# Optimization experiments

Measured on AMD Instinct MI355X. Metric: run time of the kernel, lower is better.

Reference implementation:

```python
import jax, jax.numpy as jnp
import numpy as np

EPS = 1e-5

def conv3x3(x, w, b):
    # x: [B,C,H,W], w: [O,I,3,3], padding=1 (SAME)
    y = jax.lax.conv_general_dilated(x, w, window_strides=(1, 1),
                                     padding=[(1, 1), (1, 1)],
                                     dimension_numbers=('NCHW', 'OIHW', 'NCHW'))
    return y + b[None, :, None, None]

def pool_block(x, k):
    # exact adaptive avg pool: 300 is divisible by the output size, block size k
    B, C, H, W = x.shape
    return x.reshape(B, C, H // k, k, W // k, k).mean(axis=(3, 5))

def upsample_nearest(x, k):
    # equivalent to the nested python-loop slice-assign in RIA
    return jnp.repeat(jnp.repeat(x, k, axis=2), k, axis=3)

def _conv_param(key, o, i):
    k1, k2 = jax.random.split(key)
    fan_in = i * 9
    w = jax.random.normal(k1, (o, i, 3, 3), jnp.float32) * np.sqrt(2.0 / fan_in)
    b = jax.random.normal(k2, (o,), jnp.float32) * 0.01
    return w, b

def setup_inputs() -> dict:
    key = jax.random.key(0)
    ks = jax.random.split(key, 16)
    inp = {}
    inp['im'] = jax.random.normal(ks[0], (32, 3, 300, 300), jnp.float32)
    inp['w1'], inp['b1'] = _conv_param(ks[1], 8, 3)
    inp['w2'], inp['b2'] = _conv_param(ks[2], 16, 8)
    inp['w3'], inp['b3'] = _conv_param(ks[3], 32, 16)
    inp['w4'], inp['b4'] = _conv_param(ks[4], 16, 32)
    inp['w5'], inp['b5'] = _conv_param(ks[5], 8, 16)
    inp['wc5'], inp['bc5'] = _conv_param(ks[6], 8, 16)
    inp['wc10'], inp['bc10'] = _conv_param(ks[7], 8, 16)
    inp['wc15'], inp['bc15'] = _conv_param(ks[8], 8, 16)
    inp['wg'], inp['bg'] = _conv_param(ks[9], 8, 24)
    inp['wm'], inp['bm'] = _conv_param(ks[10], 8, 24)
    inp['bn_w'] = jnp.ones((8,), jnp.float32)
    inp['bn_b'] = jnp.zeros((8,), jnp.float32)
    inp['w11'], inp['b11'] = _conv_param(ks[11], 1, 8)
    inp['gamma'] = jnp.full((1,), 0.3, jnp.float32)
    return inp

def reference(im, w1, b1, w2, b2, w3, b3, w4, b4, w5, b5,
              wc5, bc5, wc10, bc10, wc15, bc15,
              wg, bg, wm, bm, bn_w, bn_b, w11, b11, gamma):
    # attention conv chain 3->8->16->32->16->8
    x = conv3x3(im, w1, b1)
    x = conv3x3(x, w2, b2)
    x = conv3x3(x, w3, b3)
    x = conv3x3(x, w4, b4)
    x = conv3x3(x, w5, b5)  # [B,8,300,300]

    # RIA: triple-scale pooled context, nearest-upsampled and fused
    up5 = upsample_nearest(pool_block(x, 5), 5)
    up10 = upsample_nearest(pool_block(x, 10), 10)
    up15 = upsample_nearest(pool_block(x, 15), 15)
    c5 = conv3x3(jnp.concatenate([x, up5], axis=1), wc5, bc5)
    c10 = conv3x3(jnp.concatenate([x, up10], axis=1), wc10, bc10)
    c15 = conv3x3(jnp.concatenate([x, up15], axis=1), wc15, bc15)
    g_in = jnp.concatenate([c5, c10, c15], axis=1)  # [B,24,300,300]

    # gated conv (activation=None): conv(x) * sigmoid(mask_conv(x)), then BN (batch stats)
    gated = conv3x3(g_in, wg, bg) * jax.nn.sigmoid(conv3x3(g_in, wm, bm))
    mean = gated.mean(axis=(0, 2, 3), keepdims=True)
    var = gated.var(axis=(0, 2, 3), keepdims=True)
    gated = (gated - mean) * jax.lax.rsqrt(var + EPS)
    gated = gated * bn_w[None, :, None, None] + bn_b[None, :, None, None]

    # 8->1 conv, sigmoid attention map, residual gating with gamma
    att = jax.nn.sigmoid(conv3x3(gated, w11, b11))  # [B,1,300,300]
    out = gamma * (att * im) + (1.0 - gamma) * im
    return out
```

## Files before the change

### kernel.cpp

```cpp
#include <hip/hip_runtime.h>
#include <hip/hip_bf16.h>
#include <math.h>

typedef __hip_bfloat16 bf16;
typedef __attribute__((ext_vector_type(8))) __bf16 bf16x8;
typedef __attribute__((ext_vector_type(8))) unsigned short u16x8;
typedef __attribute__((ext_vector_type(4))) float f32x4;

#define H_ 300
#define W_ 300
#define HW_ 90000
#define NBATCH 32
#define NPART (NBATCH * 190)
#define NPB 95

__device__ __forceinline__ float b2f(unsigned short u) {
    return __uint_as_float((unsigned int)u << 16);
}
__device__ __forceinline__ unsigned short f2u(float v) {
    bf16 b = __float2bfloat16(v);
    return *reinterpret_cast<unsigned short*>(&b);
}
__device__ __forceinline__ float sigm(float x) { return 1.f / (1.f + __expf(-x)); }
__device__ __forceinline__ unsigned int packbf(float a, float b) {
    unsigned int r;
    asm("v_cvt_pk_bf16_f32 %0, %1, %2" : "=v"(r) : "v"(a), "v"(b));
    return r;
}
__device__ __forceinline__ void async_cp16(void* lds_base, const void* g) {
    __builtin_amdgcn_global_load_lds(
        (const __attribute__((address_space(1))) unsigned int*)g,
        (__attribute__((address_space(3))) unsigned int*)lds_base, 16, 0, 0);
}

__global__ void pack_all_k(
    const float* __restrict__ w1, const float* __restrict__ w2,
    const float* __restrict__ w3, const float* __restrict__ w4,
    const float* __restrict__ w5, const float* __restrict__ wc5,
    const float* __restrict__ wc10, const float* __restrict__ wc15,
    const float* __restrict__ wg, const float* __restrict__ wm,
    unsigned short* __restrict__ WP)
{
    const float *a = nullptr, *bsec = nullptr;
    int cs = 999, CO = 0, CI = 0, CP = 8, NS = 3, NG = 1, off = 0, special = 0;
    switch (blockIdx.x) {
        case 0: a = w2;  CO = 16; CI = 8;  CP = 8;  NS = 3; off = 0;     break;
        case 1: a = w3;  CO = 32; CI = 16; CP = 16; NS = 5; NG = 2; off = 2048;  break;
        case 2: a = w4;  CO = 16; CI = 32; CP = 32; NS = 9; off = 8192;  break;
        case 3: a = w5;  CO = 8;  CI = 16; CP = 16; NS = 5; off = 13312; break;
        case 4: special = 1; CO = 32; CI = 32; CP = 32; NS = 9; NG = 2;
                off = 16384; break;
        case 5: a = wg; bsec = wm; cs = 8; CO = 16; CI = 24; CP = 32; NS = 9;
                off = 25600; break;
        case 6: a = w1;  CO = 8;  CI = 3;  CP = 8;  NS = 3; off = 30720; break;
    }
    unsigned short* outp = WP + off;
    int TPK = 32 / CP;
    int total = NS * NG * 512;
    for (int idx = threadIdx.x; idx < total; idx += 256) {
        int j = idx & 7;
        int lane = (idx >> 3) & 63;
        int g = (idx >> 9) % NG;
        int s = idx / (512 * NG);
        int col = lane & 15, kg = lane >> 4;
        int kk = kg * 8 + j;
        int tt = kk / CP, ci = kk % CP;
        int tap = s * TPK + tt;
        float v = 0.f;
        if (special) {
            int o = ci >> 3, c8 = ci & 7;
            int convid = (g == 0) ? (col < 8 ? 0 : 1) : (col < 8 ? 2 : -1);
            if (tap < 9 && convid >= 0) {
                const float* wc = (convid == 0) ? wc5 : (convid == 1) ? wc10 : wc15;
                int colc = col & 7;
                if (o == 0) v = wc[(colc * 16 + c8) * 9 + tap];
                else if (o == convid + 1) v = wc[(colc * 16 + 8 + c8) * 9 + tap];
            }
        } else {
            int co = g * 16 + col;
            if (tap < 9 && ci < CI && co < CO)
                v = (co >= cs) ? bsec[((co - cs) * CI + ci) * 9 + tap]
                               : a[(co * CI + ci) * 9 + tap];
        }
        outp[idx] = f2u(v);
    }
}

__global__ __launch_bounds__(256) void fused12_k(
    const float* __restrict__ im, const unsigned short* __restrict__ wp1,
    const float* __restrict__ b1, const unsigned short* __restrict__ wp2,
    const float* __restrict__ b2, unsigned short* __restrict__ out)
{
    __shared__ __align__(16) unsigned short s_im[1296 * 8];
    __shared__ __align__(16) unsigned short s_x1[1156 * 8];

    int b = blockIdx.z;
    int x0 = blockIdx.x * 32, y0 = blockIdx.y * 32;
    int tid = threadIdx.x;
    int lane = tid & 63, wv = tid >> 6;
    int col = lane & 15, kg = lane >> 4;

    const float* sf = im + (size_t)b * 3 * HW_;
    bool interior = (x0 >= 2) && (x0 + 34 < W_) && (y0 >= 2) && (y0 + 34 < H_);
    if (interior) {
        const float* sf0 = sf + (size_t)(y0 - 2) * W_ + (x0 - 2);
        for (int e = tid; e < 1296; e += 256) {
            int y = e / 36;
            size_t o = (size_t)e + (size_t)y * 264;
            u16x8 v = {0, 0, 0, 0, 0, 0, 0, 0};
            v[0] = f2u(sf0[o]);
            v[1] = f2u(sf0[HW_ + o]);
            v[2] = f2u(sf0[2 * HW_ + o]);
            *(u16x8*)&s_im[e * 8] = v;
        }
    } else {
        for (int e = tid; e < 1296; e += 256) {
            int y = e / 36, x = e - y * 36;
            int gy = y0 + y - 2, gx = x0 + x - 2;
            u16x8 v = {0, 0, 0, 0, 0, 0, 0, 0};
            if (gy >= 0 && gy < H_ && gx >= 0 && gx < W_) {
                size_t o = (size_t)gy * W_ + gx;
                v[0] = f2u(sf[o]);
                v[1] = f2u(sf[HW_ + o]);
                v[2] = f2u(sf[2 * HW_ + o]);
            }
            *(u16x8*)&s_im[e * 8] = v;
        }
    }

    bf16x8 bw1[3], bw2[3];
#pragma unroll
    for (int s = 0; s < 3; ++s) {
        bw1[s] = *(const bf16x8*)&wp1[(s * 64 + lane) * 8];
        bw2[s] = *(const bf16x8*)&wp2[(s * 64 + lane) * 8];
    }

    int offs1[3], offs2[3];
#pragma unroll
    for (int s = 0; s < 3; ++s) {
        int t = s * 4 + kg;
        if (t > 8) t = 8;
        offs1[s] = ((t / 3) * 36 + (t % 3)) * 8;
        offs2[s] = ((t / 3) * 34 + (t % 3)) * 8;
    }

    float b1r[4], b2r[4];
#pragma unroll
    for (int r = 0; r < 4; ++r) {
        int co1 = kg * 4 + r;
        b1r[r] = (co1 < 8) ? b1[co1] : 0.f;
        b2r[r] = b2[kg * 4 + r];
    }

    __syncthreads();

    for (int r = wv; r < 34; r += 4) {
#pragma unroll
        for (int cg = 0; cg < 3; ++cg) {
            int base = (r * 36 + cg * 16 + col) * 8;
            f32x4 acc = {0.f, 0.f, 0.f, 0.f};
#pragma unroll
            for (int s = 0; s < 3; ++s) {
                bf16x8 a = *(const bf16x8*)&s_im[base + offs1[s]];
                acc = __builtin_amdgcn_mfma_f32_16x16x32_bf16(bw1[s], a, acc, 0, 0, 0);
            }
            int c = cg * 16 + col;
            if (kg < 2 && c < 34) {
                int gy = y0 - 1 + r, gx = x0 - 1 + c;
                bool ok = (gy >= 0) && (gy < H_) && (gx >= 0) && (gx < W_);
                float o0 = ok ? acc.x + b1r[0] : 0.f;
                float o1 = ok ? acc.y + b1r[1] : 0.f;
                float o2 = ok ? acc.z + b1r[2] : 0.f;
                float o3 = ok ? acc.w + b1r[3] : 0.f;
                uint2 st;
                st.x = packbf(o0, o1);
                st.y = packbf(o2, o3);
                *(uint2*)&s_x1[(r * 34 + c) * 8 + kg * 4] = st;
            }
        }
    }
    __syncthreads();

#pragma unroll
    for (int i = 0; i < 16; ++i) {
        int m = wv * 16 + i;
        int my = m >> 1, tx = m & 1;
        int gy = y0 + my;
        if (gy >= H_) continue;
        int base = (my * 34 + tx * 16 + col) * 8;

        f32x4 acc = {0.f, 0.f, 0.f, 0.f};
#pragma unroll
        for (int s = 0; s < 3; ++s) {
            bf16x8 a = *(const bf16x8*)&s_x1[base + offs2[s]];
            acc = __builtin_amdgcn_mfma_f32_16x16x32_bf16(bw2[s], a, acc, 0, 0, 0);
        }

        int gxx = x0 + tx * 16 + col;
        if (gxx < W_) {
            uint2 st;
            st.x = packbf(acc.x + b2r[0], acc.y + b2r[1]);
            st.y = packbf(acc.z + b2r[2], acc.w + b2r[3]);
            *(uint2*)&out[((size_t)b * HW_ + (size_t)gy * W_ + gxx) * 16 +
                          kg * 4] = st;
        }
    }
}

template <int CIN, int CINP, int COUT, int NGI, int MODE, int TH>
__global__ __launch_bounds__(256) void mfconv_k(
    const unsigned short* __restrict__ src,
    const unsigned short* __restrict__ wpack,
    const float* __restrict__ bias0, const float* __restrict__ bias1,
    unsigned short* __restrict__ out, int co_total, int co_off,
    float2* __restrict__ bnp, int img_base)
{
    constexpr int TPK = 32 / CINP;
    constexpr int NSTEP = (9 + TPK - 1) / TPK;
    constexpr int OCT = CINP / 8;
    constexpr int NPX = (TH + 2) * 34;
    constexpr int STRIDE = 256 / OCT;

    __shared__ __align__(16) unsigned short s_in[OCT * NPX * 8];

    int b = blockIdx.z;
    int x0 = blockIdx.x * 32, y0 = blockIdx.y * TH;
    int tid = threadIdx.x;
    int lane = tid & 63, wv = tid >> 6;
    bool interior = (x0 >= 1) && (x0 + 32 < W_) && (y0 >= 1) && (y0 + TH < H_);

    int oct = (OCT == 1) ? 0 : (wv % OCT);
    int phase = (OCT == 4) ? 0 : (wv / OCT);
    bool voct = (CIN == CINP) || (oct * 8 < CIN);

    {
        const unsigned short* sb = src + (size_t)b * CIN * HW_;
        if (interior) {
            if (voct) {
                const unsigned short* sb0 =
                    sb + ((size_t)(y0 - 1) * W_ + (x0 - 1)) * CIN + oct * 8;
#pragma unroll
                for (int pxb = 0; pxb < NPX; pxb += STRIDE) {
                    int base = phase * 64 + pxb;
                    if (base >= NPX) break;
                    int px = base + lane;
                    if (px < NPX) {
                        int y = px / 34;
                        async_cp16(&s_in[(oct * NPX + base) * 8],
                                   &sb0[(size_t)(px + y * 266) * CIN]);
                    }
                }
            } else {
                u16x8 z8 = {0, 0, 0, 0, 0, 0, 0, 0};
                for (int px = lane + phase * 64; px < NPX; px += STRIDE)
                    *(u16x8*)&s_in[(oct * NPX + px) * 8] = z8;
            }
        } else {
            for (int px = lane + phase * 64; px < NPX; px += STRIDE) {
                int y = px / 34, x = px - y * 34;
                int gy = y0 + y - 1, gx = x0 + x - 1;
                u16x8 v = {0, 0, 0, 0, 0, 0, 0, 0};
                if (gy >= 0 && gy < H_ && gx >= 0 && gx < W_ && voct)
                    v = *(const u16x8*)&sb[((size_t)gy * W_ + gx) * CIN + oct * 8];
                *(u16x8*)&s_in[(oct * NPX + px) * 8] = v;
            }
        }
    }

    bf16x8 bw[NGI][NSTEP];
#pragma unroll
    for (int gi = 0; gi < NGI; ++gi)
#pragma unroll
        for (int s = 0; s < NSTEP; ++s)
            bw[gi][s] = *(const bf16x8*)&wpack[((s * NGI + gi) * 64 + lane) * 8];

    int col = lane & 15, kg = lane >> 4;

    float bias_r[NGI][4];
#pragma unroll
    for (int gi = 0; gi < NGI; ++gi)
#pragma unroll
        for (int r = 0; r < 4; ++r) {
            if (MODE == 2)
                bias_r[0][r] = (kg < 2) ? bias0[kg * 4 + r] : bias1[(kg - 2) * 4 + r];
            else {
                int co_l = gi * 16 + kg * 4 + r;
                bias_r[gi][r] = (co_l < COUT) ? bias0[co_l] : 0.f;
            }
        }

    float bs[4] = {0.f, 0.f, 0.f, 0.f}, bs2[4] = {0.f, 0.f, 0.f, 0.f};

    __syncthreads();

    if constexpr (OCT == 4) {
        int myb = wv * (TH / 4);
#pragma unroll
        for (int tx = 0; tx < 2; ++tx) {
            int pbase = kg * NPX + tx * 16 + col;
            bf16x8 fr[3][3];
#pragma unroll
            for (int r = 0; r < 2; ++r)
#pragma unroll
                for (int dx = 0; dx < 3; ++dx)
                    fr[r][dx] =
                        *(const bf16x8*)&s_in[(pbase + (myb + r) * 34 + dx) * 8];
#pragma unroll
            for (int ii = 0; ii < TH / 4; ++ii) {
#pragma unroll
                for (int dx = 0; dx < 3; ++dx)
                    fr[(ii + 2) % 3][dx] =
                        *(const bf16x8*)&s_in[(pbase + (myb + ii + 2) * 34 + dx) * 8];

                f32x4 acc[NGI];
#pragma unroll
                for (int gi = 0; gi < NGI; ++gi) acc[gi] = {0.f, 0.f, 0.f, 0.f};
#pragma unroll
                for (int dy = 0; dy < 3; ++dy)
#pragma unroll
                    for (int dx = 0; dx < 3; ++dx) {
                        bf16x8 a = fr[(ii + dy) % 3][dx];
#pragma unroll
                        for (int gi = 0; gi < NGI; ++gi)
                            acc[gi] = __builtin_amdgcn_mfma_f32_16x16x32_bf16(
                                bw[gi][dy * 3 + dx], a, acc[gi], 0, 0, 0);
                    }

                int gy = y0 + myb + ii;
                int gxx = x0 + tx * 16 + col;
                if (gy < H_) {
                    if (MODE == 2) {
                        float v0 = acc[0].x + bias_r[0][0];
                        float v1 = acc[0].y + bias_r[0][1];
                        float v2 = acc[0].z + bias_r[0][2];
                        float v3 = acc[0].w + bias_r[0][3];
                        float m0 = __shfl_xor(v0, 32), m1 = __shfl_xor(v1, 32);
                        float m2 = __shfl_xor(v2, 32), m3 = __shfl_xor(v3, 32);
                        if (kg < 2 && gxx < W_) {
                            float o0 = v0 * sigm(m0), o1 = v1 * sigm(m1);
                            float o2 = v2 * sigm(m2), o3 = v3 * sigm(m3);
                            uint2 st;
                            st.x = packbf(o0, o1);
                            st.y = packbf(o2, o3);
                            *(uint2*)&out[(((size_t)b * HW_ + (size_t)gy * W_ +
                                            gxx) * 8) + kg * 4] = st;
                            bs[0] += o0; bs2[0] += o0 * o0;
                            bs[1] += o1; bs2[1] += o1 * o1;
                            bs[2] += o2; bs2[2] += o2 * o2;
                            bs[3] += o3; bs2[3] += o3 * o3;
                        }
                    } else {
#pragma unroll
                        for (int gi = 0; gi < NGI; ++gi) {
                            int co_g = gi * 16 + kg * 4;
                            if (co_g < COUT && gxx < W_) {
                                uint2 st;
                                st.x = packbf(acc[gi].x + bias_r[gi][0],
                                              acc[gi].y + bias_r[gi][1]);
                                st.y = packbf(acc[gi].z + bias_r[gi][2],
                                              acc[gi].w + bias_r[gi][3]);
                                *(uint2*)&out[((size_t)b * HW_ +
                                               (size_t)gy * W_ + gxx) *
                                                  co_total + co_off + co_g] = st;
                            }
                        }
                    }
                }
            }
        }
    } else {
        int offs[NSTEP];
#pragma unroll
        for (int s = 0; s < NSTEP; ++s) {
            int t = s * TPK + kg / OCT;
            if (t > 8) t = 8;
            offs[s] = ((t / 3) * 34 + (t % 3)) * 8 + (kg % OCT) * (NPX * 8);
        }

#pragma unroll
        for (int i = 0; i < TH / 2; ++i) {
            int m = wv * (TH / 2) + i;
            int my = m >> 1, tx = m & 1;
            int gy = y0 + my;
            if (gy >= H_) continue;
            int base = (my * 34 + tx * 16 + col) * 8;

            f32x4 acc[NGI];
#pragma unroll
            for (int gi = 0; gi < NGI; ++gi) acc[gi] = {0.f, 0.f, 0.f, 0.f};
#pragma unroll
            for (int s = 0; s < NSTEP; ++s) {
                bf16x8 a = *(const bf16x8*)&s_in[base + offs[s]];
#pragma unroll
                for (int gi = 0; gi < NGI; ++gi)
                    acc[gi] = __builtin_amdgcn_mfma_f32_16x16x32_bf16(
                        bw[gi][s], a, acc[gi], 0, 0, 0);
            }

            int gxx = x0 + tx * 16 + col;
#pragma unroll
            for (int gi = 0; gi < NGI; ++gi) {
                int co_g = gi * 16 + kg * 4;
                if (co_g < COUT && gxx < W_) {
                    uint2 st;
                    st.x = packbf(acc[gi].x + bias_r[gi][0],
                                  acc[gi].y + bias_r[gi][1]);
                    st.y = packbf(acc[gi].z + bias_r[gi][2],
                                  acc[gi].w + bias_r[gi][3]);
                    *(uint2*)&out[((size_t)b * HW_ + (size_t)gy * W_ + gxx) *
                                      co_total + co_off + co_g] = st;
                }
            }
        }
    }

    if constexpr (MODE == 2) {
#pragma unroll
        for (int off = 1; off < 16; off <<= 1) {
#pragma unroll
            for (int r = 0; r < 4; ++r) {
                bs[r] += __shfl_xor(bs[r], off);
                bs2[r] += __shfl_xor(bs2[r], off);
            }
        }
        __shared__ float bsum[4][8], bsq[4][8];
        if (lane == 0) {
#pragma unroll
            for (int r = 0; r < 4; ++r) { bsum[wv][r] = bs[r]; bsq[wv][r] = bs2[r]; }
        }
        if (lane == 16) {
#pragma unroll
            for (int r = 0; r < 4; ++r) {
                bsum[wv][4 + r] = bs[r];
                bsq[wv][4 + r] = bs2[r];
            }
        }
        __syncthreads();
        if (tid < 8) {
            float s = 0.f, s2 = 0.f;
#pragma unroll
            for (int w = 0; w < 4; ++w) { s += bsum[w][tid]; s2 += bsq[w][tid]; }
            int bIdx = (img_base + b) * 190 + blockIdx.y * 10 + blockIdx.x;
            bnp[(size_t)bIdx * 8 + tid] = make_float2(s, s2);
        }
    }
}

__global__ __launch_bounds__(256) void convc3_k(
    const unsigned short* __restrict__ src,
    const unsigned short* __restrict__ p5, const unsigned short* __restrict__ p10,
    const unsigned short* __restrict__ p15,
    const unsigned short* __restrict__ wpack,
    const float* __restrict__ bc5, const float* __restrict__ bc10,
    const float* __restrict__ bc15, unsigned short* __restrict__ out)
{
    constexpr int TH = 16;
    constexpr int NPX = (TH + 2) * 34;
    __shared__ __align__(16) unsigned short s_in[4 * NPX * 8];

    int b = blockIdx.z;
    int x0 = blockIdx.x * 32, y0 = blockIdx.y * TH;
    int tid = threadIdx.x;
    int lane = tid & 63, wv = tid >> 6;
    bool interior = (x0 >= 1) && (x0 + 32 < W_) && (y0 >= 1) && (y0 + TH < H_);

    const unsigned short* sb = src + (size_t)b * 8 * HW_;
    const unsigned short* pb5 = p5 + (size_t)b * 8 * 3600;
    const unsigned short* pb10 = p10 + (size_t)b * 8 * 900;
    const unsigned short* pb15 = p15 + (size_t)b * 8 * 400;

    int oct = wv;
    if (interior) {
        if (oct == 0) {
            const unsigned short* sb0 =
                sb + ((size_t)(y0 - 1) * W_ + (x0 - 1)) * 8;
#pragma unroll
            for (int base = 0; base < NPX; base += 64) {
                int px = base + lane;
                if (px < NPX) {
                    int y = px / 34;
                    async_cp16(&s_in[(size_t)base * 8],
                               &sb0[(size_t)(px + y * 266) * 8]);
                }
            }
        } else {
            for (int px = lane; px < NPX; px += 64) {
                int y = px / 34, x = px - y * 34;
                int gy = y0 - 1 + y, gx = x0 - 1 + x;
                const unsigned short* pp =
                    (oct == 1) ? &pb5[((size_t)(gy / 5) * 60 + gx / 5) * 8]
                    : (oct == 2) ? &pb10[((size_t)(gy / 10) * 30 + gx / 10) * 8]
                                 : &pb15[((size_t)(gy / 15) * 20 + gx / 15) * 8];
                *(u16x8*)&s_in[(oct * NPX + px) * 8] = *(const u16x8*)pp;
            }
        }
    } else {
        for (int px = lane; px < NPX; px += 64) {
            int y = px / 34, x = px - y * 34;
            int gy = y0 + y - 1, gx = x0 + x - 1;
            u16x8 v = {0, 0, 0, 0, 0, 0, 0, 0};
            if (gy >= 0 && gy < H_ && gx >= 0 && gx < W_) {
                if (oct == 0)
                    v = *(const u16x8*)&sb[((size_t)gy * W_ + gx) * 8];
                else if (oct == 1)
                    v = *(const u16x8*)&pb5[((size_t)(gy / 5) * 60 + gx / 5) * 8];
                else if (oct == 2)
                    v = *(const u16x8*)&pb10[((size_t)(gy / 10) * 30 + gx / 10) * 8];
                else
                    v = *(const u16x8*)&pb15[((size_t)(gy / 15) * 20 + gx / 15) * 8];
            }
            *(u16x8*)&s_in[(oct * NPX + px) * 8] = v;
        }
    }

    bf16x8 bw[2][9];
#pragma unroll
    for (int g = 0; g < 2; ++g)
#pragma unroll
        for (int s = 0; s < 9; ++s)
            bw[g][s] = *(const bf16x8*)&wpack[((s * 2 + g) * 64 + lane) * 8];

    int col = lane & 15, kg = lane >> 4;
    float bias_r[2][4];
#pragma unroll
    for (int r = 0; r < 4; ++r) {
        bias_r[0][r] = (kg < 2) ? bc5[kg * 4 + r] : bc10[(kg - 2) * 4 + r];
        bias_r[1][r] = (kg < 2) ? bc15[kg * 4 + r] : 0.f;
    }

    __syncthreads();

    int myb = wv * (TH / 4);
#pragma unroll
    for (int tx = 0; tx < 2; ++tx) {
        int pbase = kg * NPX + tx * 16 + col;
        bf16x8 fr[3][3];
#pragma unroll
        for (int r = 0; r < 2; ++r)
#pragma unroll
            for (int dx = 0; dx < 3; ++dx)
                fr[r][dx] = *(const bf16x8*)&s_in[(pbase + (myb + r) * 34 + dx) * 8];
#pragma unroll
        for (int ii = 0; ii < TH / 4; ++ii) {
#pragma unroll
            for (int dx = 0; dx < 3; ++dx)
                fr[(ii + 2) % 3][dx] =
                    *(const bf16x8*)&s_in[(pbase + (myb + ii + 2) * 34 + dx) * 8];

            f32x4 acc[2];
            acc[0] = {0.f, 0.f, 0.f, 0.f};
            acc[1] = {0.f, 0.f, 0.f, 0.f};
#pragma unroll
            for (int dy = 0; dy < 3; ++dy)
#pragma unroll
                for (int dx = 0; dx < 3; ++dx) {
                    bf16x8 a = fr[(ii + dy) % 3][dx];
                    acc[0] = __builtin_amdgcn_mfma_f32_16x16x32_bf16(
                        bw[0][dy * 3 + dx], a, acc[0], 0, 0, 0);
                    acc[1] = __builtin_amdgcn_mfma_f32_16x16x32_bf16(
                        bw[1][dy * 3 + dx], a, acc[1], 0, 0, 0);
                }

            int gy = y0 + myb + ii;
            int gxx = x0 + tx * 16 + col;
            if (gy < H_ && gxx < W_) {
                size_t pxo = ((size_t)b * HW_ + (size_t)gy * W_ + gxx) * 24;
                uint2 st0;
                st0.x = packbf(acc[0].x + bias_r[0][0], acc[0].y + bias_r[0][1]);
                st0.y = packbf(acc[0].z + bias_r[0][2], acc[0].w + bias_r[0][3]);
                *(uint2*)&out[pxo + kg * 4] = st0;
                if (kg < 2) {
                    uint2 st1;
                    st1.x = packbf(acc[1].x + bias_r[1][0], acc[1].y + bias_r[1][1]);
                    st1.y = packbf(acc[1].z + bias_r[1][2], acc[1].w + bias_r[1][3]);
                    *(uint2*)&out[pxo + 16 + kg * 4] = st1;
                }
            }
        }
    }
}

__global__ __launch_bounds__(256) void pool5_k(const unsigned short* __restrict__ x,
                                               unsigned short* __restrict__ p5,
                                               int n)
{
    int idx = blockIdx.x * 256 + threadIdx.x;
    if (idx >= n) return;
    int b = idx / 3600;
    int rem = idx - b * 3600;
    int i = rem / 60, j = rem - i * 60;
    const unsigned short* src =
        x + ((size_t)b * HW_ + (size_t)(i * 5) * W_ + j * 5) * 8;
    float ss[8] = {0, 0, 0, 0, 0, 0, 0, 0};
#pragma unroll
    for (int r = 0; r < 5; ++r)
#pragma unroll
        for (int c = 0; c < 5; ++c) {
            u16x8 v = *(const u16x8*)&src[((size_t)r * W_ + c) * 8];
#pragma unroll
            for (int k = 0; k < 8; ++k) ss[k] += b2f(v[k]);
        }
    uint4 st;
    st.x = packbf(ss[0] * 0.04f, ss[1] * 0.04f);
    st.y = packbf(ss[2] * 0.04f, ss[3] * 0.04f);
    st.z = packbf(ss[4] * 0.04f, ss[5] * 0.04f);
    st.w = packbf(ss[6] * 0.04f, ss[7] * 0.04f);
    *(uint4*)&p5[(size_t)idx * 8] = st;
}

template <int R, int OD>
__device__ __forceinline__ void poolr_body(const unsigned short* __restrict__ p5,
                                           unsigned short* __restrict__ po, int idx)
{
    int b = idx / (OD * OD);
    int rem = idx - b * OD * OD;
    int i = rem / OD, j = rem - i * OD;
    const unsigned short* src =
        p5 + ((size_t)b * 3600 + (size_t)(i * R) * 60 + j * R) * 8;
    float ss[8] = {0, 0, 0, 0, 0, 0, 0, 0};
    const float inv = 1.f / (R * R);
#pragma unroll
    for (int r = 0; r < R; ++r)
#pragma unroll
        for (int c = 0; c < R; ++c) {
            u16x8 v = *(const u16x8*)&src[((size_t)r * 60 + c) * 8];
#pragma unroll
            for (int k = 0; k < 8; ++k) ss[k] += b2f(v[k]);
        }
    uint4 st;
    st.x = packbf(ss[0] * inv, ss[1] * inv);
    st.y = packbf(ss[2] * inv, ss[3] * inv);
    st.z = packbf(ss[4] * inv, ss[5] * inv);
    st.w = packbf(ss[6] * inv, ss[7] * inv);
    *(uint4*)&po[(size_t)idx * 8] = st;
}

__global__ __launch_bounds__(256) void poolrs_k(const unsigned short* __restrict__ p5,
                                                unsigned short* __restrict__ p10,
                                                unsigned short* __restrict__ p15,
                                                int n10, int n15)
{
    int idx = blockIdx.x * 256 + threadIdx.x;
    if (idx < n10) {
        poolr_body<2, 30>(p5, p10, idx);
    } else {
        idx -= n10;
        if (idx < n15) poolr_body<3, 20>(p5, p15, idx);
    }
}

__global__ __launch_bounds__(256) void reduce_parts_k(
    const float2* __restrict__ parts, float2* __restrict__ parts2)
{
    int k = blockIdx.x;
    int tid = threadIdx.x;
    int c = tid & 7, j = tid >> 3;
    float s = 0.f, s2 = 0.f;
    for (int r = j; r < NPB; r += 32) {
        float2 p = parts[((size_t)k * NPB + r) * 8 + c];
        s += p.x;
        s2 += p.y;
    }
    __shared__ float2 red[256];
    red[tid] = make_float2(s, s2);
    __syncthreads();
    if (tid < 8) {
        float a = 0.f, b = 0.f;
        for (int q = 0; q < 32; ++q) {
            float2 p = red[q * 8 + tid];
            a += p.x;
            b += p.y;
        }
        parts2[(size_t)k * 8 + tid] = make_float2(a, b);
    }
}

__global__ __launch_bounds__(256) void stats_fold_k(
    const float2* __restrict__ parts2, const float* __restrict__ bn_w,
    const float* __restrict__ bn_b, const float* __restrict__ w11,
    const float* __restrict__ b11, float* __restrict__ wfold)
{
    __shared__ float sc[8], tc[8];
    __shared__ float2 acc8[8];
    int tid = threadIdx.x;
    int c = tid >> 5, sl = tid & 31;
    float s = 0.f, s2 = 0.f;
    for (int i = sl; i < 64; i += 32) {
        float2 p = parts2[(size_t)i * 8 + c];
        s += p.x;
        s2 += p.y;
    }
#pragma unroll
    for (int off = 16; off > 0; off >>= 1) {
        s += __shfl_down(s, off, 32);
        s2 += __shfl_down(s2, off, 32);
    }
    if (sl == 0) acc8[c] = make_float2(s, s2);
    __syncthreads();
    if (tid < 8) {
        double ds = acc8[tid].x, ds2 = acc8[tid].y;
        double N = (double)NBATCH * HW_;
        double mean = ds / N;
        double var = ds2 / N - mean * mean;
        float rstd = (float)(1.0 / sqrt(var + 1e-5));
        float scv = bn_w[tid] * rstd;
        sc[tid] = scv;
        tc[tid] = bn_b[tid] - (float)mean * scv;
    }
    __syncthreads();
    if (tid < 72) {
        int t = tid >> 3, ci = tid & 7;
        wfold[tid] = w11[ci * 9 + t] * sc[ci];
    }
    if (tid == 72) {
        float a = b11[0];
        for (int i = 0; i < 72; ++i) a += w11[i] * tc[i / 9];
        wfold[72] = a;
    }
}

__global__ __launch_bounds__(256) void final_k(
    const unsigned short* __restrict__ gated, const float* __restrict__ wf,
    const float* __restrict__ im, const float* __restrict__ gamma,
    float* __restrict__ out)
{
    __shared__ __align__(16) unsigned short s_g[1156 * 8];
    __shared__ float s_w[80];

    int b = blockIdx.z;
    int x0 = blockIdx.x * 32, y0 = blockIdx.y * 32;
    int tid = threadIdx.x;
    int lane = tid & 63, wv = tid >> 6;
    bool interior = (x0 >= 1) && (x0 + 32 < W_) && (y0 >= 1) && (y0 + 32 < H_);

    if (tid < 73) s_w[tid] = wf[tid];

    const unsigned short* gb = gated + (size_t)b * HW_ * 8;
    if (interior) {
        const unsigned short* gb0 = gb + ((size_t)(y0 - 1) * W_ + (x0 - 1)) * 8;
        for (int base = wv * 64; base < 1156; base += 256) {
            int px = base + lane;
            if (px < 1156) {
                int y = px / 34;
                async_cp16(&s_g[(size_t)base * 8],
                           &gb0[(size_t)(px + y * 266) * 8]);
            }
        }
    } else {
        for (int e = tid; e < 1156; e += 256) {
            int y = e / 34, x = e - y * 34;
            int gy = y0 + y - 1, gx = x0 + x - 1;
            u16x8 v = {0, 0, 0, 0, 0, 0, 0, 0};
            if (gy >= 0 && gy < H_ && gx >= 0 && gx < W_)
                v = *(const u16x8*)&gb[((size_t)gy * W_ + gx) * 8];
            *(u16x8*)&s_g[e * 8] = v;
        }
    }
    __syncthreads();

    int qx = (tid & 15) * 2, qy = (tid >> 4) * 2;
    float f[4];
    float gm = *gamma;
#pragma unroll
    for (int p = 0; p < 4; ++p) {
        int ly = qy + (p >> 1), lx = qx + (p & 1);
        float acc = s_w[72];
#pragma unroll
        for (int t = 0; t < 9; ++t) {
            u16x8 n = *(const u16x8*)&s_g[((ly + t / 3) * 34 + lx + t % 3) * 8];
#pragma unroll
            for (int ci = 0; ci < 8; ++ci) acc += b2f(n[ci]) * s_w[t * 8 + ci];
        }
        f[p] = (1.f - gm) + gm * sigm(acc);
    }

    int px = x0 + qx, py = y0 + qy;
    if (px < W_) {
#pragma unroll
        for (int ch = 0; ch < 3; ++ch) {
            const float* imb = im + ((size_t)b * 3 + ch) * HW_;
            float* ob = out + ((size_t)b * 3 + ch) * HW_;
#pragma unroll
            for (int pr = 0; pr < 2; ++pr) {
                if (py + pr < H_) {
                    float2 iv = *(const float2*)&imb[(size_t)(py + pr) * W_ + px];
                    float2 ov;
                    ov.x = iv.x * f[pr * 2 + 0];
                    ov.y = iv.y * f[pr * 2 + 1];
                    *(float2*)&ob[(size_t)(py + pr) * W_ + px] = ov;
                }
            }
        }
    }
}


extern "C" void kernel_launch(void* const* d_in, const int* in_sizes, int n_in,
                              void* d_out, int out_size, void* d_ws,
                              size_t ws_size, hipStream_t stream)
{
    (void)in_sizes; (void)n_in; (void)out_size;

    const float* im  = (const float*)d_in[0];
    const float* w1  = (const float*)d_in[1];
    const float* b1  = (const float*)d_in[2];
    const float* w2  = (const float*)d_in[3];
    const float* b2  = (const float*)d_in[4];
    const float* w3  = (const float*)d_in[5];
    const float* b3  = (const float*)d_in[6];
    const float* w4  = (const float*)d_in[7];
    const float* b4  = (const float*)d_in[8];
    const float* w5  = (const float*)d_in[9];
    const float* b5  = (const float*)d_in[10];
    const float* wc5 = (const float*)d_in[11];
    const float* bc5 = (const float*)d_in[12];
    const float* wc10= (const float*)d_in[13];
    const float* bc10= (const float*)d_in[14];
    const float* wc15= (const float*)d_in[15];
    const float* bc15= (const float*)d_in[16];
    const float* wg  = (const float*)d_in[17];
    const float* bg  = (const float*)d_in[18];
    const float* wm  = (const float*)d_in[19];
    const float* bm  = (const float*)d_in[20];
    const float* bnw = (const float*)d_in[21];
    const float* bnb = (const float*)d_in[22];
    const float* w11 = (const float*)d_in[23];
    const float* b11 = (const float*)d_in[24];
    const float* gam = (const float*)d_in[25];
    float* out = (float*)d_out;

    const size_t GATED_B = 46080000;
    const size_t PER_IMG = 1440000 + 2880000 + 5760000 + 57600 + 14400 + 6656;
    const size_t MISC    = 1048576;
    int c = 32;
    while (c > 1 && GATED_B + MISC + (size_t)c * PER_IMG + 2048 > ws_size)
        c >>= 1;

    char* p = (char*)d_ws;
    auto take = [&](size_t bytes) {
        char* r = p;
        p += (bytes + 255) & ~(size_t)255;
        return r;
    };
    unsigned short* GATED = (unsigned short*)take(GATED_B);
    unsigned short* A   = (unsigned short*)take((size_t)c * 1440000);
    unsigned short* Bb  = (unsigned short*)take((size_t)c * 2880000);
    unsigned short* C   = (unsigned short*)take((size_t)c * 5760000);
    unsigned short* P5  = (unsigned short*)take((size_t)c * 57600);
    unsigned short* P10 = (unsigned short*)take((size_t)c * 14400);
    unsigned short* P15 = (unsigned short*)take((size_t)c * 6656);
    float2* parts  = (float2*)take((size_t)NPART * 8 * sizeof(float2));
    float2* parts2 = (float2*)take(64 * 8 * sizeof(float2));
    float*  wfold  = (float*)take(512);
    unsigned short* WP = (unsigned short*)take(65536);

    unsigned short* PK2 = WP;
    unsigned short* PK3 = WP + 2048;
    unsigned short* PK4 = WP + 8192;
    unsigned short* PK5 = WP + 13312;
    unsigned short* PKc = WP + 16384;
    unsigned short* PKg = WP + 25600;
    unsigned short* PK1 = WP + 30720;

    dim3 blk(256);

    pack_all_k<<<dim3(7), blk, 0, stream>>>(w1, w2, w3, w4, w5, wc5, wc10, wc15,
                                            wg, wm, WP);

    for (int b0 = 0; b0 < NBATCH; b0 += c) {
        dim3 g32(10, 10, c);
        dim3 g16(10, 19, c);
        const float* imc = im + (size_t)b0 * 3 * HW_;

        fused12_k<<<g32, blk, 0, stream>>>(imc, PK1, b1, PK2, b2, Bb);

        mfconv_k<16, 16, 32, 2, 0, 32><<<g32, blk, 0, stream>>>(
            Bb, PK3, b3, nullptr, C, 32, 0, nullptr, 0);
        mfconv_k<32, 32, 16, 1, 0, 16><<<g16, blk, 0, stream>>>(
            C, PK4, b4, nullptr, Bb, 16, 0, nullptr, 0);
        mfconv_k<16, 16, 8, 1, 0, 32><<<g32, blk, 0, stream>>>(
            Bb, PK5, b5, nullptr, A, 8, 0, nullptr, 0);

        int n5 = c * 3600, n10 = c * 900, n15 = c * 400;
        pool5_k<<<dim3((n5 + 255) / 256), blk, 0, stream>>>(A, P5, n5);
        poolrs_k<<<dim3((n10 + n15 + 255) / 256), blk, 0, stream>>>(P5, P10, P15,
                                                                    n10, n15);

        convc3_k<<<g16, blk, 0, stream>>>(A, P5, P10, P15, PKc, bc5, bc10, bc15, C);

        mfconv_k<24, 32, 16, 1, 2, 16><<<g16, blk, 0, stream>>>(
            C, PKg, bg, bm, GATED + (size_t)b0 * HW_ * 8, 8, 0, parts, b0);
    }

    reduce_parts_k<<<dim3(64), blk, 0, stream>>>(parts, parts2);
    stats_fold_k<<<dim3(1), blk, 0, stream>>>(parts2, bnw, bnb, w11, b11, wfold);
    final_k<<<dim3(10, 10, NBATCH), blk, 0, stream>>>(GATED, wfold, im, gam,
                                                      out);
}
```

Baseline: 413.1 us.

## Read pooled context from compact shared tables instead of materialized upsampled tiles

The multi-scale conv kernel no longer expands each pooled map into a full upsampled tile in shared memory. It stores only the small block of pooled cells covering the tile, and computes each pixel's table index with a multiply-shift division plus a zero sentinel for padding. The freed shared memory allows the tile height to grow from 16 to 32 rows, halving the grid and the halo overhead. In exchange, the inner loop does more index arithmetic per fragment load, and the lanes of one wave read the same few table entries.

```diff
diff --git a/kernel.cpp b/kernel.cpp
--- a/kernel.cpp
+++ b/kernel.cpp
@@ -446,6 +446,13 @@
     }
 }
 
+#define C3_NPX 1156
+#define C3_T5  0
+#define C3_T10 72
+#define C3_T15 97
+#define C3_SENT 113
+#define C3_TBL 120
+
 __global__ __launch_bounds__(256) void convc3_k(
     const unsigned short* __restrict__ src,
     const unsigned short* __restrict__ p5, const unsigned short* __restrict__ p10,
@@ -454,9 +461,8 @@
     const float* __restrict__ bc5, const float* __restrict__ bc10,
     const float* __restrict__ bc15, unsigned short* __restrict__ out)
 {
-    constexpr int TH = 16;
-    constexpr int NPX = (TH + 2) * 34;
-    __shared__ __align__(16) unsigned short s_in[4 * NPX * 8];
+    constexpr int TH = 32;
+    __shared__ __align__(16) unsigned short s_all[(C3_NPX + C3_TBL) * 8];
 
     int b = blockIdx.z;
     int x0 = blockIdx.x * 32, y0 = blockIdx.y * TH;
@@ -469,48 +475,56 @@
     const unsigned short* pb10 = p10 + (size_t)b * 8 * 900;
     const unsigned short* pb15 = p15 + (size_t)b * 8 * 400;
 
-    int oct = wv;
+    int ylo = (y0 - 1 < 0) ? 0 : y0 - 1;
+    int xlo = (x0 - 1 < 0) ? 0 : x0 - 1;
+    int yb5 = ylo / 5, xb5 = xlo / 5;
+    int yb10 = ylo / 10, xb10 = xlo / 10;
+    int yb15 = ylo / 15, xb15 = xlo / 15;
+
     if (interior) {
-        if (oct == 0) {
-            const unsigned short* sb0 =
-                sb + ((size_t)(y0 - 1) * W_ + (x0 - 1)) * 8;
-#pragma unroll
-            for (int base = 0; base < NPX; base += 64) {
-                int px = base + lane;
-                if (px < NPX) {
-                    int y = px / 34;
-                    async_cp16(&s_in[(size_t)base * 8],
-                               &sb0[(size_t)(px + y * 266) * 8]);
-                }
-            }
-        } else {
-            for (int px = lane; px < NPX; px += 64) {
-                int y = px / 34, x = px - y * 34;
-                int gy = y0 - 1 + y, gx = x0 - 1 + x;
-                const unsigned short* pp =
-                    (oct == 1) ? &pb5[((size_t)(gy / 5) * 60 + gx / 5) * 8]
-                    : (oct == 2) ? &pb10[((size_t)(gy / 10) * 30 + gx / 10) * 8]
-                                 : &pb15[((size_t)(gy / 15) * 20 + gx / 15) * 8];
-                *(u16x8*)&s_in[(oct * NPX + px) * 8] = *(const u16x8*)pp;
+        const unsigned short* sb0 = sb + ((size_t)(y0 - 1) * W_ + (x0 - 1)) * 8;
+        for (int base = wv * 64; base < C3_NPX; base += 256) {
+            int px = base + lane;
+            if (px < C3_NPX) {
+                int y = px / 34;
+                async_cp16(&s_all[(size_t)base * 8],
+                           &sb0[(size_t)(px + y * 266) * 8]);
             }
         }
     } else {
-        for (int px = lane; px < NPX; px += 64) {
+        for (int px = tid; px < C3_NPX; px += 256) {
             int y = px / 34, x = px - y * 34;
             int gy = y0 + y - 1, gx = x0 + x - 1;
             u16x8 v = {0, 0, 0, 0, 0, 0, 0, 0};
-            if (gy >= 0 && gy < H_ && gx >= 0 && gx < W_) {
-                if (oct == 0)
-                    v = *(const u16x8*)&sb[((size_t)gy * W_ + gx) * 8];
-                else if (oct == 1)
-                    v = *(const u16x8*)&pb5[((size_t)(gy / 5) * 60 + gx / 5) * 8];
-                else if (oct == 2)
-                    v = *(const u16x8*)&pb10[((size_t)(gy / 10) * 30 + gx / 10) * 8];
-                else
-                    v = *(const u16x8*)&pb15[((size_t)(gy / 15) * 20 + gx / 15) * 8];
-            }
-            *(u16x8*)&s_in[(oct * NPX + px) * 8] = v;
-        }
+            if (gy >= 0 && gy < H_ && gx >= 0 && gx < W_)
+                v = *(const u16x8*)&sb[((size_t)gy * W_ + gx) * 8];
+            *(u16x8*)&s_all[px * 8] = v;
+        }
+    }
+
+    if (tid < 72) {
+        int r = tid / 9, cc = tid - r * 9;
+        int yi = yb5 + r; if (yi > 59) yi = 59;
+        int xi = xb5 + cc; if (xi > 59) xi = 59;
+        *(u16x8*)&s_all[(C3_NPX + C3_T5 + tid) * 8] =
+            *(const u16x8*)&pb5[((size_t)yi * 60 + xi) * 8];
+    } else if (tid < 97) {
+        int t = tid - 72;
+        int r = t / 5, cc = t - r * 5;
+        int yi = yb10 + r; if (yi > 29) yi = 29;
+        int xi = xb10 + cc; if (xi > 29) xi = 29;
+        *(u16x8*)&s_all[(C3_NPX + C3_T10 + t) * 8] =
+            *(const u16x8*)&pb10[((size_t)yi * 30 + xi) * 8];
+    } else if (tid < 113) {
+        int t = tid - 97;
+        int r = t / 4, cc = t - r * 4;
+        int yi = yb15 + r; if (yi > 19) yi = 19;
+        int xi = xb15 + cc; if (xi > 19) xi = 19;
+        *(u16x8*)&s_all[(C3_NPX + C3_T15 + t) * 8] =
+            *(const u16x8*)&pb15[((size_t)yi * 20 + xi) * 8];
+    } else if (tid == 113) {
+        u16x8 z = {0, 0, 0, 0, 0, 0, 0, 0};
+        *(u16x8*)&s_all[(C3_NPX + C3_SENT) * 8] = z;
     }
 
     bf16x8 bw[2][9];
@@ -528,24 +542,61 @@
         bias_r[1][r] = (kg < 2) ? bc15[kg * 4 + r] : 0.f;
     }
 
+    unsigned int M = (kg == 1) ? 13108u : (kg == 2) ? 6554u : 4370u;
+    int ybk = (kg == 1) ? yb5 : (kg == 2) ? yb10 : yb15;
+    int xbk = (kg == 1) ? xb5 : (kg == 2) ? xb10 : xb15;
+    int TWk = (kg == 1) ? 9 : (kg == 2) ? 5 : 4;
+    int tbk = C3_NPX + ((kg == 1) ? C3_T5 : (kg == 2) ? C3_T10 : C3_T15);
+
     __syncthreads();
 
     int myb = wv * (TH / 4);
 #pragma unroll
     for (int tx = 0; tx < 2; ++tx) {
-        int pbase = kg * NPX + tx * 16 + col;
+        int pbx = tx * 16 + col;
+        int gx0 = x0 - 1 + pbx;
+        int xrel[3];
+        bool xok[3];
+#pragma unroll
+        for (int dx = 0; dx < 3; ++dx) {
+            int gx = gx0 + dx;
+            xok[dx] = ((unsigned)gx < (unsigned)W_);
+            int gxc = gx < 0 ? 0 : gx;
+            xrel[dx] = (int)(((unsigned)gxc * M) >> 16) - xbk;
+        }
+
+        auto frag_off = [&](int r, int dx, int prow, bool yok) -> int {
+            if (kg == 0) return (r * 34 + pbx + dx) * 8;
+            bool ok = yok && xok[dx];
+            return ok ? (prow + xrel[dx]) * 8 : (C3_NPX + C3_SENT) * 8;
+        };
+        auto row_prow = [&](int r, bool& yok) -> int {
+            int gy = y0 - 1 + r;
+            yok = ((unsigned)gy < (unsigned)H_);
+            int gyc = gy < 0 ? 0 : gy;
+            int yidx = (int)(((unsigned)gyc * M) >> 16);
+            return tbk + (yidx - ybk) * TWk;
+        };
+
         bf16x8 fr[3][3];
 #pragma unroll
-        for (int r = 0; r < 2; ++r)
+        for (int r = 0; r < 2; ++r) {
+            bool yok;
+            int prow = row_prow(myb + r, yok);
 #pragma unroll
             for (int dx = 0; dx < 3; ++dx)
-                fr[r][dx] = *(const bf16x8*)&s_in[(pbase + (myb + r) * 34 + dx) * 8];
+                fr[r][dx] = *(const bf16x8*)&s_all[frag_off(myb + r, dx, prow, yok)];
+        }
 #pragma unroll
         for (int ii = 0; ii < TH / 4; ++ii) {
-#pragma unroll
-            for (int dx = 0; dx < 3; ++dx)
-                fr[(ii + 2) % 3][dx] =
-                    *(const bf16x8*)&s_in[(pbase + (myb + ii + 2) * 34 + dx) * 8];
+            {
+                bool yok;
+                int prow = row_prow(myb + ii + 2, yok);
+#pragma unroll
+                for (int dx = 0; dx < 3; ++dx)
+                    fr[(ii + 2) % 3][dx] =
+                        *(const bf16x8*)&s_all[frag_off(myb + ii + 2, dx, prow, yok)];
+            }
 
             f32x4 acc[2];
             acc[0] = {0.f, 0.f, 0.f, 0.f};
@@ -886,7 +937,7 @@
         poolrs_k<<<dim3((n10 + n15 + 255) / 256), blk, 0, stream>>>(P5, P10, P15,
                                                                     n10, n15);
 
-        convc3_k<<<g16, blk, 0, stream>>>(A, P5, P10, P15, PKc, bc5, bc10, bc15, C);
+        convc3_k<<<g32, blk, 0, stream>>>(A, P5, P10, P15, PKc, bc5, bc10, bc15, C);
 
         mfconv_k<24, 32, 16, 1, 2, 16><<<g16, blk, 0, stream>>>(
             C, PKg, bg, bm, GATED + (size_t)b0 * HW_ * 8, 8, 0, parts, b0);
```

Measured after the change: 404.4 us. 2.1% less time.
